# Performance work log

Hardware: AMD Instinct MI355X
Metric: run time of the kernel (lower is better)

Reference implementation:

```python
import jax, jax.numpy as jnp
import numpy as np

D_MODEL = 1024
N_HEADS = 16
HEAD_DIM = D_MODEL // N_HEADS


def setup_inputs() -> dict:
    key = jax.random.key(0)
    k_x, k_qkv, k_out = jax.random.split(key, 3)
    x = jax.random.normal(k_x, (2, 2048, D_MODEL), dtype=jnp.float32)
    # torch Linear weight is [out, in]; store transposed for x @ W
    w_qkv = jax.random.normal(k_qkv, (D_MODEL, 3 * D_MODEL), dtype=jnp.float32) * (1.0 / np.sqrt(D_MODEL))
    w_out = jax.random.normal(k_out, (D_MODEL, D_MODEL), dtype=jnp.float32) * (1.0 / np.sqrt(D_MODEL))
    return {"x": x, "w_qkv": w_qkv, "w_out": w_out}


def reference(x, w_qkv, w_out):
    B, T, C = x.shape
    qkv = x @ w_qkv  # [B, T, 3C]
    q, k, v = jnp.split(qkv, 3, axis=-1)

    def reshape(t):
        return t.reshape(B, T, N_HEADS, HEAD_DIM).transpose(0, 2, 1, 3)  # [B,H,T,hd]

    q, k, v = reshape(q), reshape(k), reshape(v)
    scale = 1.0 / jnp.sqrt(jnp.asarray(HEAD_DIM, dtype=x.dtype))
    attn = jnp.einsum('bhqd,bhkd->bhqk', q, k) * scale  # [B,H,T,T]
    causal = jnp.tril(jnp.ones((T, T), dtype=bool))
    attn = jnp.where(causal, attn, -jnp.inf)
    attn = jax.nn.softmax(attn, axis=-1)
    out = jnp.einsum('bhqk,bhkd->bhqd', attn, v)  # [B,H,T,hd]
    out = out.transpose(0, 2, 1, 3).reshape(B, T, C)
    return out @ w_out
```

## Files before the change

### kernel.cpp

```cpp
#include <hip/hip_runtime.h>
#include <hip/hip_bf16.h>
#include <stdint.h>

typedef __bf16 bf16x8 __attribute__((ext_vector_type(8)));
typedef float  f32x4  __attribute__((ext_vector_type(4)));
typedef unsigned short ushort8 __attribute__((ext_vector_type(8)));

#define DEVI static __device__ __forceinline__

static constexpr int TB  = 2;
static constexpr int TT  = 2048;
static constexpr int TC  = 1024;
static constexpr int TH  = 16;
static constexpr int THD = 64;
static constexpr int TM  = TB * TT;

DEVI unsigned short f2bu(float f) {
  union { float f; unsigned u; } v; v.f = f;
  unsigned u = v.u;
  return (unsigned short)((u + 0x7FFFu + ((u >> 16) & 1u)) >> 16);
}

DEVI void gload_lds16(const unsigned short* g, char* l) {
  __builtin_amdgcn_global_load_lds((const __attribute__((address_space(1))) void*)g,
                                   (__attribute__((address_space(3))) void*)l, 16, 0, 0);
}

__global__ void cast_bf16_kernel(const float* __restrict__ in, unsigned short* __restrict__ out, int n8) {
  int i = blockIdx.x * blockDim.x + threadIdx.x;
  if (i >= n8) return;
  float4 a = ((const float4*)in)[2 * i];
  float4 b = ((const float4*)in)[2 * i + 1];
  ushort8 r;
  r[0] = f2bu(a.x); r[1] = f2bu(a.y); r[2] = f2bu(a.z); r[3] = f2bu(a.w);
  r[4] = f2bu(b.x); r[5] = f2bu(b.y); r[6] = f2bu(b.z); r[7] = f2bu(b.w);
  ((ushort8*)out)[i] = r;
}

__global__ void transpose_cast_kernel(const float* __restrict__ in, unsigned short* __restrict__ out,
                                      int R, int Cc) {
  __shared__ float tile[32][33];
  const int c0 = blockIdx.x * 32, r0 = blockIdx.y * 32;
  const int tx = threadIdx.x, ty = threadIdx.y;
#pragma unroll
  for (int i = 0; i < 4; ++i)
    tile[ty + i * 8][tx] = in[(size_t)(r0 + ty + i * 8) * Cc + c0 + tx];
  __syncthreads();
#pragma unroll
  for (int i = 0; i < 4; ++i)
    out[(size_t)(c0 + ty + i * 8) * R + r0 + tx] = f2bu(tile[tx][ty + i * 8]);
}

__global__ void transpose_v_kernel(const unsigned short* __restrict__ Vh, unsigned short* __restrict__ Vt) {
  __shared__ unsigned short tile[64][72];
  const int t0 = blockIdx.x * 64;
  const size_t ho = (size_t)(blockIdx.z * TH + blockIdx.y) * TT * THD;
  const int tid = threadIdx.x;
#pragma unroll
  for (int it = 0; it < 2; ++it) {
    const int r = it * 32 + (tid >> 3), c8 = tid & 7;
    *(ushort8*)&tile[r][c8 * 8] = *(const ushort8*)(Vh + ho + (size_t)(t0 + r) * THD + c8 * 8);
  }
  __syncthreads();
  const int d = tid >> 2, tc = tid & 3;
  ushort8 a, b;
#pragma unroll
  for (int j = 0; j < 8; ++j) a[j] = tile[tc * 16 + j][d];
#pragma unroll
  for (int j = 0; j < 8; ++j) b[j] = tile[tc * 16 + 8 + j][d];
  *(ushort8*)(Vt + ho + (size_t)d * TT + t0 + tc * 16) = a;
  *(ushort8*)(Vt + ho + (size_t)d * TT + t0 + tc * 16 + 8) = b;
}

template <int EPI>
__launch_bounds__(256)
__global__ void gemm_bt_kernel(const unsigned short* __restrict__ A, const unsigned short* __restrict__ Bt,
                               float* __restrict__ Cf,
                               unsigned short* __restrict__ Qo, unsigned short* __restrict__ Ko,
                               unsigned short* __restrict__ Vo,
                               int Mm, int Nn, int Kk) {
  __shared__ __align__(16) char smem[32768];
  char* ldsA = smem;
  char* ldsB = smem + 16384;
  const int tid = threadIdx.x;
  const int lane = tid & 63;
  const int wave = tid >> 6;
  const int l15 = lane & 15, l4 = lane >> 4;
  const int m0 = blockIdx.y * 128;
  const int n0 = blockIdx.x * 128;
  const int wm = (wave >> 1) * 64;
  const int wn = (wave & 1) * 64;

  f32x4 acc[4][4];
#pragma unroll
  for (int a = 0; a < 4; ++a)
#pragma unroll
    for (int b = 0; b < 4; ++b) acc[a][b] = (f32x4){0.f, 0.f, 0.f, 0.f};

  const int nk = Kk >> 6;
  for (int kt = 0; kt < nk; ++kt) {
    __syncthreads();
#pragma unroll
    for (int r = 0; r < 4; ++r) {
      const int cid = r * 256 + tid;
      const int row = cid >> 3;
      const int srcc = (cid & 7) ^ (row & 7);
      gload_lds16(A + (size_t)(m0 + row) * Kk + kt * 64 + srcc * 8, ldsA + (r * 256 + wave * 64) * 16);
      gload_lds16(Bt + (size_t)(n0 + row) * Kk + kt * 64 + srcc * 8, ldsB + (r * 256 + wave * 64) * 16);
    }
    __syncthreads();
#pragma unroll
    for (int ks = 0; ks < 2; ++ks) {
      bf16x8 af[4], bfv[4];
#pragma unroll
      for (int mf = 0; mf < 4; ++mf) {
        const int row = wm + mf * 16 + l15;
        const int ch = (ks * 4 + l4) ^ (row & 7);
        af[mf] = *(const bf16x8*)(ldsA + row * 128 + ch * 16);
      }
#pragma unroll
      for (int nf = 0; nf < 4; ++nf) {
        const int row = wn + nf * 16 + l15;
        const int ch = (ks * 4 + l4) ^ (row & 7);
        bfv[nf] = *(const bf16x8*)(ldsB + row * 128 + ch * 16);
      }
#pragma unroll
      for (int mf = 0; mf < 4; ++mf)
#pragma unroll
        for (int nf = 0; nf < 4; ++nf)
          acc[mf][nf] = __builtin_amdgcn_mfma_f32_16x16x32_bf16(af[mf], bfv[nf], acc[mf][nf], 0, 0, 0);
    }
  }

  if constexpr (EPI == 0) {
#pragma unroll
    for (int mf = 0; mf < 4; ++mf)
#pragma unroll
      for (int nf = 0; nf < 4; ++nf)
#pragma unroll
        for (int i = 0; i < 4; ++i) {
          const int row = m0 + wm + mf * 16 + l4 * 4 + i;
          const int col = n0 + wn + nf * 16 + l15;
          Cf[(size_t)row * Nn + col] = acc[mf][nf][i];
        }
  } else {
#pragma unroll
    for (int mf = 0; mf < 4; ++mf)
#pragma unroll
      for (int nf = 0; nf < 4; ++nf)
#pragma unroll
        for (int i = 0; i < 4; ++i) {
          const int row = m0 + wm + mf * 16 + l4 * 4 + i;
          const int col = n0 + wn + nf * 16 + l15;
          const int sel = col >> 10;
          const int wi = col & 1023;
          const int h = wi >> 6;
          const int d = wi & 63;
          const int b = row >> 11;
          const int t = row & 2047;
          float v = acc[mf][nf][i];
          if (sel == 0) v *= 0.125f;
          unsigned short* dst = (sel == 0) ? Qo : (sel == 1) ? Ko : Vo;
          dst[((size_t)(b * TH + h) * TT + t) * THD + d] = f2bu(v);
        }
  }
}

__launch_bounds__(256)
__global__ void attn_kernel(const unsigned short* __restrict__ Qp, const unsigned short* __restrict__ Kp,
                            const unsigned short* __restrict__ Vt, unsigned short* __restrict__ Op) {
  __shared__ __align__(16) char smem[49152];
  const int tid = threadIdx.x;
  const int lane = tid & 63;
  const int wave = tid >> 6;
  char* ldsP = smem + 32768 + wave * 4096;
  const int l15 = lane & 15, l4 = lane >> 4;

  const int h = blockIdx.y;
  const int b = blockIdx.z;
  const int bxe = (int)blockIdx.x ^ (b ? 15 : 0);
  const int qA = 31 - bxe;
  const int qB = bxe;
  const size_t headoff = (size_t)(b * TH + h) * TT * THD;
  const int qt = (wave >> 1) ? qB : qA;
  const int q0 = qt * 64 + (wave & 1) * 32;
  const int ntile = qA + 1;

  bf16x8 aq[2][2];
#pragma unroll
  for (int mf = 0; mf < 2; ++mf)
#pragma unroll
    for (int ks = 0; ks < 2; ++ks)
      aq[mf][ks] = *(const bf16x8*)(Qp + headoff + (size_t)(q0 + mf * 16 + l15) * THD + ks * 32 + l4 * 8);

  f32x4 o[2][4];
  float mrun[2][4], lrun[2][4];
#pragma unroll
  for (int mf = 0; mf < 2; ++mf) {
#pragma unroll
    for (int nd = 0; nd < 4; ++nd) o[mf][nd] = (f32x4){0.f, 0.f, 0.f, 0.f};
#pragma unroll
    for (int i = 0; i < 4; ++i) { mrun[mf][i] = -3.0e38f; lrun[mf][i] = 0.f; }
  }

  auto stage = [&](int kt, int c) {
    const int kv0 = kt * 64;
    char* bK = smem + c * 16384;
    char* bV = bK + 8192;
#pragma unroll
    for (int r = 0; r < 2; ++r) {
      const int cid = r * 256 + tid;
      const int row = cid >> 3;
      const int srcc = (cid & 7) ^ (row & 7);
      gload_lds16(Kp + headoff + (size_t)(kv0 + row) * THD + srcc * 8, bK + (r * 256 + wave * 64) * 16);
      gload_lds16(Vt + headoff + (size_t)row * TT + kv0 + srcc * 8, bV + (r * 256 + wave * 64) * 16);
    }
  };

  int cur = 0;
  stage(0, 0);
  for (int kt = 0; kt < ntile; ++kt) {
    const int kv0 = kt * 64;
    if (kt + 1 < ntile) {
      stage(kt + 1, cur ^ 1);
      asm volatile("s_waitcnt vmcnt(4)" ::: "memory");
    } else {
      asm volatile("s_waitcnt vmcnt(0)" ::: "memory");
    }
    __builtin_amdgcn_s_barrier();
    __builtin_amdgcn_sched_barrier(0);
    char* ldsK = smem + cur * 16384;
    char* ldsV = ldsK + 8192;

    if (kv0 <= q0 + 31) {
      f32x4 s[2][4];
#pragma unroll
      for (int mf = 0; mf < 2; ++mf)
#pragma unroll
        for (int nf = 0; nf < 4; ++nf) s[mf][nf] = (f32x4){0.f, 0.f, 0.f, 0.f};
#pragma unroll
      for (int ks = 0; ks < 2; ++ks) {
        bf16x8 bk[4];
#pragma unroll
        for (int nf = 0; nf < 4; ++nf) {
          const int row = nf * 16 + l15;
          const int ch = (ks * 4 + l4) ^ (row & 7);
          bk[nf] = *(const bf16x8*)(ldsK + row * 128 + ch * 16);
        }
#pragma unroll
        for (int mf = 0; mf < 2; ++mf)
#pragma unroll
          for (int nf = 0; nf < 4; ++nf)
            s[mf][nf] = __builtin_amdgcn_mfma_f32_16x16x32_bf16(aq[mf][ks], bk[nf], s[mf][nf], 0, 0, 0);
      }

      if (kv0 + 63 > q0) {
#pragma unroll
        for (int mf = 0; mf < 2; ++mf)
#pragma unroll
          for (int nf = 0; nf < 4; ++nf)
#pragma unroll
            for (int i = 0; i < 4; ++i) {
              const int rq = q0 + mf * 16 + l4 * 4 + i;
              const int ck = kv0 + nf * 16 + l15;
              if (ck > rq) s[mf][nf][i] = -3.0e38f;
            }
      }

      float mt[2][4], alpha[2][4], rs[2][4];
#pragma unroll
      for (int mf = 0; mf < 2; ++mf)
#pragma unroll
        for (int i = 0; i < 4; ++i) {
          float m = fmaxf(fmaxf(s[mf][0][i], s[mf][1][i]), fmaxf(s[mf][2][i], s[mf][3][i]));
#pragma unroll
          for (int d = 1; d < 16; d <<= 1) m = fmaxf(m, __shfl_xor(m, d));
          const float mn = fmaxf(mrun[mf][i], m);
          alpha[mf][i] = __expf(mrun[mf][i] - mn);
          mrun[mf][i] = mn;
          mt[mf][i] = mn;
          rs[mf][i] = 0.f;
        }
#pragma unroll
      for (int mf = 0; mf < 2; ++mf)
#pragma unroll
        for (int nf = 0; nf < 4; ++nf)
#pragma unroll
          for (int i = 0; i < 4; ++i) {
            const float p = __expf(s[mf][nf][i] - mt[mf][i]);
            rs[mf][i] += p;
            const int row = mf * 16 + l4 * 4 + i;
            const int col = nf * 16 + l15;
            *(unsigned short*)(ldsP + row * 128 + (((col >> 3) ^ (row & 7)) << 4) + ((col & 7) << 1)) = f2bu(p);
          }
#pragma unroll
      for (int mf = 0; mf < 2; ++mf)
#pragma unroll
        for (int i = 0; i < 4; ++i) {
#pragma unroll
          for (int d = 1; d < 16; d <<= 1) rs[mf][i] += __shfl_xor(rs[mf][i], d);
          lrun[mf][i] = lrun[mf][i] * alpha[mf][i] + rs[mf][i];
        }
#pragma unroll
      for (int mf = 0; mf < 2; ++mf)
#pragma unroll
        for (int nd = 0; nd < 4; ++nd)
#pragma unroll
          for (int i = 0; i < 4; ++i) o[mf][nd][i] *= alpha[mf][i];

      asm volatile("s_waitcnt lgkmcnt(0)" ::: "memory");

#pragma unroll
      for (int ks2 = 0; ks2 < 2; ++ks2) {
        bf16x8 pa[2];
#pragma unroll
        for (int mf = 0; mf < 2; ++mf) {
          const int row = mf * 16 + l15;
          const int ch = (ks2 * 4 + l4) ^ (row & 7);
          pa[mf] = *(const bf16x8*)(ldsP + row * 128 + ch * 16);
        }
#pragma unroll
        for (int nf = 0; nf < 4; ++nf) {
          const int row = nf * 16 + l15;
          const int ch = (ks2 * 4 + l4) ^ (row & 7);
          const bf16x8 bv = *(const bf16x8*)(ldsV + row * 128 + ch * 16);
#pragma unroll
          for (int mf = 0; mf < 2; ++mf)
            o[mf][nf] = __builtin_amdgcn_mfma_f32_16x16x32_bf16(pa[mf], bv, o[mf][nf], 0, 0, 0);
        }
      }
    }

    __builtin_amdgcn_s_barrier();
    cur ^= 1;
  }

#pragma unroll
  for (int mf = 0; mf < 2; ++mf)
#pragma unroll
    for (int nd = 0; nd < 4; ++nd)
#pragma unroll
      for (int i = 0; i < 4; ++i) {
        const int row = q0 + mf * 16 + l4 * 4 + i;
        const int col = h * THD + nd * 16 + l15;
        Op[(size_t)(b * TT + row) * TC + col] = f2bu(o[mf][nd][i] / lrun[mf][i]);
      }
}

extern "C" void kernel_launch(void* const* d_in, const int* in_sizes, int n_in,
                              void* d_out, int out_size, void* d_ws, size_t ws_size,
                              hipStream_t stream) {
  (void)in_sizes; (void)n_in; (void)out_size; (void)ws_size;
  const float* x = (const float*)d_in[0];
  const float* wqkv = (const float*)d_in[1];
  const float* wout = (const float*)d_in[2];
  char* ws = (char*)d_ws;
  unsigned short* Xb = (unsigned short*)(ws);
  unsigned short* Wq = (unsigned short*)(ws + ((size_t)8 << 20));
  unsigned short* Wo = (unsigned short*)(ws + ((size_t)14 << 20));
  unsigned short* Qh = (unsigned short*)(ws + ((size_t)16 << 20));
  unsigned short* Kh = (unsigned short*)(ws + ((size_t)24 << 20));
  unsigned short* Vh = (unsigned short*)(ws + ((size_t)32 << 20));
  unsigned short* Oh = (unsigned short*)(ws + ((size_t)40 << 20));
  unsigned short* Vtp = Xb;
  float* out = (float*)d_out;

  cast_bf16_kernel<<<2048, 256, 0, stream>>>(x, Xb, TM * TC / 8);
  transpose_cast_kernel<<<dim3(96, 32), dim3(32, 8), 0, stream>>>(wqkv, Wq, TC, 3 * TC);
  transpose_cast_kernel<<<dim3(32, 32), dim3(32, 8), 0, stream>>>(wout, Wo, TC, TC);
  gemm_bt_kernel<1><<<dim3(24, 32), 256, 0, stream>>>(Xb, Wq, nullptr, Qh, Kh, Vh, TM, 3 * TC, TC);
  transpose_v_kernel<<<dim3(32, 16, 2), 256, 0, stream>>>(Vh, Vtp);
  attn_kernel<<<dim3(16, 16, 2), 256, 0, stream>>>(Qh, Kh, Vtp, Oh);
  gemm_bt_kernel<0><<<dim3(8, 32), 256, 0, stream>>>(Oh, Wo, out, nullptr, nullptr, nullptr, TM, TC, TC);
}
```

Before: 238.8 us.

## Stage 128-wide KV tiles per barrier in attention and raise MFMA priority

The attention kernel now loads K and V in 128-key tiles, double-buffered in 64KB of LDS, and processes each tile as two 64-key sub-blocks. This halves the number of barrier and wait pairs per block and issues larger global-to-LDS batches. The V tile layout and swizzle change to a 256-byte row stride. s_setprio calls are placed around the MFMA sections. The larger LDS footprint (80KB) may lower how many blocks fit per CU.

```diff
diff --git a/kernel.cpp b/kernel.cpp
--- a/kernel.cpp
+++ b/kernel.cpp
@@ -169,11 +169,11 @@
 __launch_bounds__(256)
 __global__ void attn_kernel(const unsigned short* __restrict__ Qp, const unsigned short* __restrict__ Kp,
                             const unsigned short* __restrict__ Vt, unsigned short* __restrict__ Op) {
-  __shared__ __align__(16) char smem[49152];
+  __shared__ __align__(16) char smem[81920];
   const int tid = threadIdx.x;
   const int lane = tid & 63;
   const int wave = tid >> 6;
-  char* ldsP = smem + 32768 + wave * 4096;
+  char* ldsP = smem + 65536 + wave * 4096;
   const int l15 = lane & 15, l4 = lane >> 4;
 
   const int h = blockIdx.y;
@@ -184,7 +184,7 @@
   const size_t headoff = (size_t)(b * TH + h) * TT * THD;
   const int qt = (wave >> 1) ? qB : qA;
   const int q0 = qt * 64 + (wave & 1) * 32;
-  const int ntile = qA + 1;
+  const int ntile = (qA + 2) >> 1;
 
   bf16x8 aq[2][2];
 #pragma unroll
@@ -204,129 +204,139 @@
   }
 
   auto stage = [&](int kt, int c) {
-    const int kv0 = kt * 64;
-    char* bK = smem + c * 16384;
-    char* bV = bK + 8192;
-#pragma unroll
-    for (int r = 0; r < 2; ++r) {
+    const int kv0 = kt * 128;
+    char* bK = smem + c * 32768;
+    char* bV = bK + 16384;
+#pragma unroll
+    for (int r = 0; r < 4; ++r) {
       const int cid = r * 256 + tid;
-      const int row = cid >> 3;
-      const int srcc = (cid & 7) ^ (row & 7);
-      gload_lds16(Kp + headoff + (size_t)(kv0 + row) * THD + srcc * 8, bK + (r * 256 + wave * 64) * 16);
-      gload_lds16(Vt + headoff + (size_t)row * TT + kv0 + srcc * 8, bV + (r * 256 + wave * 64) * 16);
+      const int krow = cid >> 3;
+      const int kcol = (cid & 7) ^ (krow & 7);
+      gload_lds16(Kp + headoff + (size_t)(kv0 + krow) * THD + kcol * 8, bK + (r * 256 + wave * 64) * 16);
+      const int vrow = cid >> 4;
+      const int vcol = (cid & 8) | ((cid ^ vrow) & 7);
+      gload_lds16(Vt + headoff + (size_t)vrow * TT + kv0 + vcol * 8, bV + (r * 256 + wave * 64) * 16);
     }
   };
 
   int cur = 0;
   stage(0, 0);
   for (int kt = 0; kt < ntile; ++kt) {
-    const int kv0 = kt * 64;
     if (kt + 1 < ntile) {
       stage(kt + 1, cur ^ 1);
-      asm volatile("s_waitcnt vmcnt(4)" ::: "memory");
+      asm volatile("s_waitcnt vmcnt(8)" ::: "memory");
     } else {
       asm volatile("s_waitcnt vmcnt(0)" ::: "memory");
     }
     __builtin_amdgcn_s_barrier();
     __builtin_amdgcn_sched_barrier(0);
-    char* ldsK = smem + cur * 16384;
-    char* ldsV = ldsK + 8192;
-
-    if (kv0 <= q0 + 31) {
-      f32x4 s[2][4];
-#pragma unroll
-      for (int mf = 0; mf < 2; ++mf)
-#pragma unroll
-        for (int nf = 0; nf < 4; ++nf) s[mf][nf] = (f32x4){0.f, 0.f, 0.f, 0.f};
-#pragma unroll
-      for (int ks = 0; ks < 2; ++ks) {
-        bf16x8 bk[4];
-#pragma unroll
-        for (int nf = 0; nf < 4; ++nf) {
-          const int row = nf * 16 + l15;
-          const int ch = (ks * 4 + l4) ^ (row & 7);
-          bk[nf] = *(const bf16x8*)(ldsK + row * 128 + ch * 16);
-        }
+    char* bK = smem + cur * 32768;
+    char* bV = bK + 16384;
+
+#pragma unroll
+    for (int sub = 0; sub < 2; ++sub) {
+      const int kvb = kt * 128 + sub * 64;
+      if (kvb <= q0 + 31) {
+        f32x4 s[2][4];
+#pragma unroll
+        for (int mf = 0; mf < 2; ++mf)
+#pragma unroll
+          for (int nf = 0; nf < 4; ++nf) s[mf][nf] = (f32x4){0.f, 0.f, 0.f, 0.f};
+#pragma unroll
+        for (int ks = 0; ks < 2; ++ks) {
+          bf16x8 bk[4];
+#pragma unroll
+          for (int nf = 0; nf < 4; ++nf) {
+            const int row = sub * 64 + nf * 16 + l15;
+            const int ch = (ks * 4 + l4) ^ (row & 7);
+            bk[nf] = *(const bf16x8*)(bK + row * 128 + ch * 16);
+          }
+          __builtin_amdgcn_s_setprio(1);
+#pragma unroll
+          for (int mf = 0; mf < 2; ++mf)
+#pragma unroll
+            for (int nf = 0; nf < 4; ++nf)
+              s[mf][nf] = __builtin_amdgcn_mfma_f32_16x16x32_bf16(aq[mf][ks], bk[nf], s[mf][nf], 0, 0, 0);
+          __builtin_amdgcn_s_setprio(0);
+        }
+
+        if (kvb + 63 > q0) {
+#pragma unroll
+          for (int mf = 0; mf < 2; ++mf)
+#pragma unroll
+            for (int nf = 0; nf < 4; ++nf)
+#pragma unroll
+              for (int i = 0; i < 4; ++i) {
+                const int rq = q0 + mf * 16 + l4 * 4 + i;
+                const int ck = kvb + nf * 16 + l15;
+                if (ck > rq) s[mf][nf][i] = -3.0e38f;
+              }
+        }
+
+        float mt[2][4], alpha[2][4], rs[2][4];
+#pragma unroll
+        for (int mf = 0; mf < 2; ++mf)
+#pragma unroll
+          for (int i = 0; i < 4; ++i) {
+            float m = fmaxf(fmaxf(s[mf][0][i], s[mf][1][i]), fmaxf(s[mf][2][i], s[mf][3][i]));
+#pragma unroll
+            for (int d = 1; d < 16; d <<= 1) m = fmaxf(m, __shfl_xor(m, d));
+            const float mn = fmaxf(mrun[mf][i], m);
+            alpha[mf][i] = __expf(mrun[mf][i] - mn);
+            mrun[mf][i] = mn;
+            mt[mf][i] = mn;
+            rs[mf][i] = 0.f;
+          }
 #pragma unroll
         for (int mf = 0; mf < 2; ++mf)
 #pragma unroll
           for (int nf = 0; nf < 4; ++nf)
-            s[mf][nf] = __builtin_amdgcn_mfma_f32_16x16x32_bf16(aq[mf][ks], bk[nf], s[mf][nf], 0, 0, 0);
-      }
-
-      if (kv0 + 63 > q0) {
-#pragma unroll
-        for (int mf = 0; mf < 2; ++mf)
-#pragma unroll
-          for (int nf = 0; nf < 4; ++nf)
 #pragma unroll
             for (int i = 0; i < 4; ++i) {
-              const int rq = q0 + mf * 16 + l4 * 4 + i;
-              const int ck = kv0 + nf * 16 + l15;
-              if (ck > rq) s[mf][nf][i] = -3.0e38f;
+              const float p = __expf(s[mf][nf][i] - mt[mf][i]);
+              rs[mf][i] += p;
+              const int row = mf * 16 + l4 * 4 + i;
+              const int col = nf * 16 + l15;
+              *(unsigned short*)(ldsP + row * 128 + (((col >> 3) ^ (row & 7)) << 4) + ((col & 7) << 1)) = f2bu(p);
             }
-      }
-
-      float mt[2][4], alpha[2][4], rs[2][4];
-#pragma unroll
-      for (int mf = 0; mf < 2; ++mf)
-#pragma unroll
-        for (int i = 0; i < 4; ++i) {
-          float m = fmaxf(fmaxf(s[mf][0][i], s[mf][1][i]), fmaxf(s[mf][2][i], s[mf][3][i]));
-#pragma unroll
-          for (int d = 1; d < 16; d <<= 1) m = fmaxf(m, __shfl_xor(m, d));
-          const float mn = fmaxf(mrun[mf][i], m);
-          alpha[mf][i] = __expf(mrun[mf][i] - mn);
-          mrun[mf][i] = mn;
-          mt[mf][i] = mn;
-          rs[mf][i] = 0.f;
-        }
-#pragma unroll
-      for (int mf = 0; mf < 2; ++mf)
-#pragma unroll
-        for (int nf = 0; nf < 4; ++nf)
+#pragma unroll
+        for (int mf = 0; mf < 2; ++mf)
 #pragma unroll
           for (int i = 0; i < 4; ++i) {
-            const float p = __expf(s[mf][nf][i] - mt[mf][i]);
-            rs[mf][i] += p;
-            const int row = mf * 16 + l4 * 4 + i;
-            const int col = nf * 16 + l15;
-            *(unsigned short*)(ldsP + row * 128 + (((col >> 3) ^ (row & 7)) << 4) + ((col & 7) << 1)) = f2bu(p);
-          }
-#pragma unroll
-      for (int mf = 0; mf < 2; ++mf)
-#pragma unroll
-        for (int i = 0; i < 4; ++i) {
-#pragma unroll
-          for (int d = 1; d < 16; d <<= 1) rs[mf][i] += __shfl_xor(rs[mf][i], d);
-          lrun[mf][i] = lrun[mf][i] * alpha[mf][i] + rs[mf][i];
-        }
-#pragma unroll
-      for (int mf = 0; mf < 2; ++mf)
-#pragma unroll
-        for (int nd = 0; nd < 4; ++nd)
-#pragma unroll
-          for (int i = 0; i < 4; ++i) o[mf][nd][i] *= alpha[mf][i];
-
-      asm volatile("s_waitcnt lgkmcnt(0)" ::: "memory");
-
-#pragma unroll
-      for (int ks2 = 0; ks2 < 2; ++ks2) {
-        bf16x8 pa[2];
-#pragma unroll
-        for (int mf = 0; mf < 2; ++mf) {
-          const int row = mf * 16 + l15;
-          const int ch = (ks2 * 4 + l4) ^ (row & 7);
-          pa[mf] = *(const bf16x8*)(ldsP + row * 128 + ch * 16);
-        }
-#pragma unroll
-        for (int nf = 0; nf < 4; ++nf) {
-          const int row = nf * 16 + l15;
-          const int ch = (ks2 * 4 + l4) ^ (row & 7);
-          const bf16x8 bv = *(const bf16x8*)(ldsV + row * 128 + ch * 16);
-#pragma unroll
-          for (int mf = 0; mf < 2; ++mf)
-            o[mf][nf] = __builtin_amdgcn_mfma_f32_16x16x32_bf16(pa[mf], bv, o[mf][nf], 0, 0, 0);
+#pragma unroll
+            for (int d = 1; d < 16; d <<= 1) rs[mf][i] += __shfl_xor(rs[mf][i], d);
+            lrun[mf][i] = lrun[mf][i] * alpha[mf][i] + rs[mf][i];
+          }
+#pragma unroll
+        for (int mf = 0; mf < 2; ++mf)
+#pragma unroll
+          for (int nd = 0; nd < 4; ++nd)
+#pragma unroll
+            for (int i = 0; i < 4; ++i) o[mf][nd][i] *= alpha[mf][i];
+
+        asm volatile("s_waitcnt lgkmcnt(0)" ::: "memory");
+
+#pragma unroll
+        for (int ks2 = 0; ks2 < 2; ++ks2) {
+          bf16x8 pa[2];
+#pragma unroll
+          for (int mf = 0; mf < 2; ++mf) {
+            const int row = mf * 16 + l15;
+            const int ch = (ks2 * 4 + l4) ^ (row & 7);
+            pa[mf] = *(const bf16x8*)(ldsP + row * 128 + ch * 16);
+          }
+          __builtin_amdgcn_s_setprio(1);
+#pragma unroll
+          for (int nf = 0; nf < 4; ++nf) {
+            const int vrow = nf * 16 + l15;
+            const int c16 = sub * 8 + ks2 * 4 + l4;
+            const int ch = (c16 & 8) | ((c16 ^ vrow) & 7);
+            const bf16x8 bv = *(const bf16x8*)(bV + vrow * 256 + ch * 16);
+#pragma unroll
+            for (int mf = 0; mf < 2; ++mf)
+              o[mf][nf] = __builtin_amdgcn_mfma_f32_16x16x32_bf16(pa[mf], bv, o[mf][nf], 0, 0, 0);
+          }
+          __builtin_amdgcn_s_setprio(0);
         }
       }
     }
```

New measurement: 244.1 us. 2.2% more time.

## Restructure attention to transposed 32x32 MFMA keeping P in registers

Applied to the files above, without the earlier changes.

Rewrites the attention inner loop to use 32x32x16 bf16 MFMAs computing S^T (K as A operand, Q as B), so each lane owns one query row and the softmax row reductions need only a single cross-half shuffle. P is packed to bf16 with v_cvt_pk_bf16_f32 and fed directly as the B operand of the PV MFMA, removing the per-wave LDS round trip for P and shrinking shared memory. It also adds a lazy rescale that skips the O/l rescaling unless the running max grows by more than 8, and vectorizes the output store. The lazy rescale depends on the fp32 accumulators tolerating unnormalized exponentials up to e^8, and V reads now use split 8-byte LDS loads.

```diff
diff --git a/kernel.cpp b/kernel.cpp
--- a/kernel.cpp
+++ b/kernel.cpp
@@ -4,7 +4,9 @@
 
 typedef __bf16 bf16x8 __attribute__((ext_vector_type(8)));
 typedef float  f32x4  __attribute__((ext_vector_type(4)));
+typedef float  f32x16 __attribute__((ext_vector_type(16)));
 typedef unsigned short ushort8 __attribute__((ext_vector_type(8)));
+typedef unsigned short ushort4v __attribute__((ext_vector_type(4)));
 
 #define DEVI static __device__ __forceinline__
 
@@ -19,6 +21,12 @@
   union { float f; unsigned u; } v; v.f = f;
   unsigned u = v.u;
   return (unsigned short)((u + 0x7FFFu + ((u >> 16) & 1u)) >> 16);
+}
+
+DEVI unsigned cvtpk(float lo, float hi) {
+  unsigned r;
+  asm("v_cvt_pk_bf16_f32 %0, %1, %2" : "=v"(r) : "v"(lo), "v"(hi));
+  return r;
 }
 
 DEVI void gload_lds16(const unsigned short* g, char* l) {
@@ -169,12 +177,11 @@
 __launch_bounds__(256)
 __global__ void attn_kernel(const unsigned short* __restrict__ Qp, const unsigned short* __restrict__ Kp,
                             const unsigned short* __restrict__ Vt, unsigned short* __restrict__ Op) {
-  __shared__ __align__(16) char smem[49152];
+  __shared__ __align__(16) char smem[32768];
   const int tid = threadIdx.x;
   const int lane = tid & 63;
   const int wave = tid >> 6;
-  char* ldsP = smem + 32768 + wave * 4096;
-  const int l15 = lane & 15, l4 = lane >> 4;
+  const int l31 = lane & 31, hi = lane >> 5;
 
   const int h = blockIdx.y;
   const int b = blockIdx.z;
@@ -185,23 +192,19 @@
   const int qt = (wave >> 1) ? qB : qA;
   const int q0 = qt * 64 + (wave & 1) * 32;
   const int ntile = qA + 1;
-
-  bf16x8 aq[2][2];
-#pragma unroll
-  for (int mf = 0; mf < 2; ++mf)
-#pragma unroll
-    for (int ks = 0; ks < 2; ++ks)
-      aq[mf][ks] = *(const bf16x8*)(Qp + headoff + (size_t)(q0 + mf * 16 + l15) * THD + ks * 32 + l4 * 8);
-
-  f32x4 o[2][4];
-  float mrun[2][4], lrun[2][4];
-#pragma unroll
-  for (int mf = 0; mf < 2; ++mf) {
-#pragma unroll
-    for (int nd = 0; nd < 4; ++nd) o[mf][nd] = (f32x4){0.f, 0.f, 0.f, 0.f};
-#pragma unroll
-    for (int i = 0; i < 4; ++i) { mrun[mf][i] = -3.0e38f; lrun[mf][i] = 0.f; }
-  }
+  const int rq = q0 + l31;
+
+  bf16x8 aq[4];
+#pragma unroll
+  for (int ks = 0; ks < 4; ++ks)
+    aq[ks] = *(const bf16x8*)(Qp + headoff + (size_t)rq * THD + ks * 16 + hi * 8);
+
+  f32x16 o[2];
+#pragma unroll
+  for (int dt = 0; dt < 2; ++dt)
+#pragma unroll
+    for (int r = 0; r < 16; ++r) o[dt][r] = 0.f;
+  float mrun = -3.0e38f, lrun = 0.f;
 
   auto stage = [&](int kt, int c) {
     const int kv0 = kt * 64;
@@ -233,118 +236,100 @@
     char* ldsV = ldsK + 8192;
 
     if (kv0 <= q0 + 31) {
-      f32x4 s[2][4];
-#pragma unroll
-      for (int mf = 0; mf < 2; ++mf)
-#pragma unroll
-        for (int nf = 0; nf < 4; ++nf) s[mf][nf] = (f32x4){0.f, 0.f, 0.f, 0.f};
-#pragma unroll
-      for (int ks = 0; ks < 2; ++ks) {
-        bf16x8 bk[4];
-#pragma unroll
-        for (int nf = 0; nf < 4; ++nf) {
-          const int row = nf * 16 + l15;
-          const int ch = (ks * 4 + l4) ^ (row & 7);
-          bk[nf] = *(const bf16x8*)(ldsK + row * 128 + ch * 16);
-        }
-#pragma unroll
-        for (int mf = 0; mf < 2; ++mf)
-#pragma unroll
-          for (int nf = 0; nf < 4; ++nf)
-            s[mf][nf] = __builtin_amdgcn_mfma_f32_16x16x32_bf16(aq[mf][ks], bk[nf], s[mf][nf], 0, 0, 0);
+      f32x16 s[2];
+#pragma unroll
+      for (int kvt = 0; kvt < 2; ++kvt) {
+#pragma unroll
+        for (int r = 0; r < 16; ++r) s[kvt][r] = 0.f;
+#pragma unroll
+        for (int ks = 0; ks < 4; ++ks) {
+          const int row = kvt * 32 + l31;
+          const int ch = (ks * 2 + hi) ^ (row & 7);
+          const bf16x8 ak = *(const bf16x8*)(ldsK + row * 128 + ch * 16);
+          s[kvt] = __builtin_amdgcn_mfma_f32_32x32x16_bf16(ak, aq[ks], s[kvt], 0, 0, 0);
+        }
       }
 
       if (kv0 + 63 > q0) {
 #pragma unroll
-        for (int mf = 0; mf < 2; ++mf)
-#pragma unroll
-          for (int nf = 0; nf < 4; ++nf)
-#pragma unroll
-            for (int i = 0; i < 4; ++i) {
-              const int rq = q0 + mf * 16 + l4 * 4 + i;
-              const int ck = kv0 + nf * 16 + l15;
-              if (ck > rq) s[mf][nf][i] = -3.0e38f;
-            }
-      }
-
-      float mt[2][4], alpha[2][4], rs[2][4];
-#pragma unroll
-      for (int mf = 0; mf < 2; ++mf)
-#pragma unroll
-        for (int i = 0; i < 4; ++i) {
-          float m = fmaxf(fmaxf(s[mf][0][i], s[mf][1][i]), fmaxf(s[mf][2][i], s[mf][3][i]));
-#pragma unroll
-          for (int d = 1; d < 16; d <<= 1) m = fmaxf(m, __shfl_xor(m, d));
-          const float mn = fmaxf(mrun[mf][i], m);
-          alpha[mf][i] = __expf(mrun[mf][i] - mn);
-          mrun[mf][i] = mn;
-          mt[mf][i] = mn;
-          rs[mf][i] = 0.f;
-        }
-#pragma unroll
-      for (int mf = 0; mf < 2; ++mf)
-#pragma unroll
-        for (int nf = 0; nf < 4; ++nf)
-#pragma unroll
-          for (int i = 0; i < 4; ++i) {
-            const float p = __expf(s[mf][nf][i] - mt[mf][i]);
-            rs[mf][i] += p;
-            const int row = mf * 16 + l4 * 4 + i;
-            const int col = nf * 16 + l15;
-            *(unsigned short*)(ldsP + row * 128 + (((col >> 3) ^ (row & 7)) << 4) + ((col & 7) << 1)) = f2bu(p);
+        for (int kvt = 0; kvt < 2; ++kvt)
+#pragma unroll
+          for (int r = 0; r < 16; ++r) {
+            const int ck = kv0 + kvt * 32 + (r & 3) + 8 * (r >> 2) + 4 * hi;
+            if (ck > rq) s[kvt][r] = -3.0e38f;
           }
-#pragma unroll
-      for (int mf = 0; mf < 2; ++mf)
-#pragma unroll
-        for (int i = 0; i < 4; ++i) {
-#pragma unroll
-          for (int d = 1; d < 16; d <<= 1) rs[mf][i] += __shfl_xor(rs[mf][i], d);
-          lrun[mf][i] = lrun[mf][i] * alpha[mf][i] + rs[mf][i];
-        }
-#pragma unroll
-      for (int mf = 0; mf < 2; ++mf)
-#pragma unroll
-        for (int nd = 0; nd < 4; ++nd)
-#pragma unroll
-          for (int i = 0; i < 4; ++i) o[mf][nd][i] *= alpha[mf][i];
-
-      asm volatile("s_waitcnt lgkmcnt(0)" ::: "memory");
-
-#pragma unroll
-      for (int ks2 = 0; ks2 < 2; ++ks2) {
-        bf16x8 pa[2];
-#pragma unroll
-        for (int mf = 0; mf < 2; ++mf) {
-          const int row = mf * 16 + l15;
-          const int ch = (ks2 * 4 + l4) ^ (row & 7);
-          pa[mf] = *(const bf16x8*)(ldsP + row * 128 + ch * 16);
-        }
-#pragma unroll
-        for (int nf = 0; nf < 4; ++nf) {
-          const int row = nf * 16 + l15;
-          const int ch = (ks2 * 4 + l4) ^ (row & 7);
-          const bf16x8 bv = *(const bf16x8*)(ldsV + row * 128 + ch * 16);
-#pragma unroll
-          for (int mf = 0; mf < 2; ++mf)
-            o[mf][nf] = __builtin_amdgcn_mfma_f32_16x16x32_bf16(pa[mf], bv, o[mf][nf], 0, 0, 0);
-        }
-      }
-    }
-
+      }
+
+      float mx = s[0][0];
+#pragma unroll
+      for (int kvt = 0; kvt < 2; ++kvt)
+#pragma unroll
+        for (int r = 0; r < 16; ++r) mx = fmaxf(mx, s[kvt][r]);
+      mx = fmaxf(mx, __shfl_xor(mx, 32));
+      if (!__all(mx <= mrun + 8.f)) {
+        const float mn = fmaxf(mrun, mx);
+        const float al = __expf(mrun - mn);
+        lrun *= al;
+#pragma unroll
+        for (int dt = 0; dt < 2; ++dt)
+#pragma unroll
+          for (int r = 0; r < 16; ++r) o[dt][r] *= al;
+        mrun = mn;
+      }
+      float rs = 0.f;
+#pragma unroll
+      for (int kvt = 0; kvt < 2; ++kvt)
+#pragma unroll
+        for (int r = 0; r < 16; ++r) {
+          const float p = __expf(s[kvt][r] - mrun);
+          s[kvt][r] = p;
+          rs += p;
+        }
+      lrun += rs + __shfl_xor(rs, 32);
+
+      bf16x8 pb[4];
+#pragma unroll
+      for (int kvt = 0; kvt < 2; ++kvt)
+#pragma unroll
+        for (int kh = 0; kh < 2; ++kh) {
+          union { unsigned u[4]; bf16x8 v; } pk;
+#pragma unroll
+          for (int w = 0; w < 4; ++w)
+            pk.u[w] = cvtpk(s[kvt][kh * 8 + 2 * w], s[kvt][kh * 8 + 2 * w + 1]);
+          pb[kvt * 2 + kh] = pk.v;
+        }
+
+#pragma unroll
+      for (int dt = 0; dt < 2; ++dt)
+#pragma unroll
+        for (int n = 0; n < 4; ++n) {
+          const int row = dt * 32 + l31;
+          const int c1 = (2 * n) ^ (row & 7);
+          const int c2 = (2 * n + 1) ^ (row & 7);
+          union { ushort4v h[2]; bf16x8 v; } av;
+          av.h[0] = *(const ushort4v*)(ldsV + row * 128 + c1 * 16 + hi * 8);
+          av.h[1] = *(const ushort4v*)(ldsV + row * 128 + c2 * 16 + hi * 8);
+          o[dt] = __builtin_amdgcn_mfma_f32_32x32x16_bf16(av.v, pb[n], o[dt], 0, 0, 0);
+        }
+    }
+
+    asm volatile("s_waitcnt lgkmcnt(0)" ::: "memory");
+    __builtin_amdgcn_sched_barrier(0);
     __builtin_amdgcn_s_barrier();
     cur ^= 1;
   }
 
-#pragma unroll
-  for (int mf = 0; mf < 2; ++mf)
-#pragma unroll
-    for (int nd = 0; nd < 4; ++nd)
-#pragma unroll
-      for (int i = 0; i < 4; ++i) {
-        const int row = q0 + mf * 16 + l4 * 4 + i;
-        const int col = h * THD + nd * 16 + l15;
-        Op[(size_t)(b * TT + row) * TC + col] = f2bu(o[mf][nd][i] / lrun[mf][i]);
-      }
+  const float inv = 1.0f / lrun;
+  unsigned short* orow = Op + (size_t)(b * TT + rq) * TC + h * THD;
+#pragma unroll
+  for (int dt = 0; dt < 2; ++dt)
+#pragma unroll
+    for (int r4 = 0; r4 < 4; ++r4) {
+      const unsigned u0 = cvtpk(o[dt][r4 * 4 + 0] * inv, o[dt][r4 * 4 + 1] * inv);
+      const unsigned u1 = cvtpk(o[dt][r4 * 4 + 2] * inv, o[dt][r4 * 4 + 3] * inv);
+      uint2 w; w.x = u0; w.y = u1;
+      *(uint2*)(orow + dt * 32 + r4 * 8 + hi * 4) = w;
+    }
 }
 
 extern "C" void kernel_launch(void* const* d_in, const int* in_sizes, int n_in,
```

After: 196.4 us. 1.22x faster.
